# Performance work log

Measured on AMD Instinct MI355X. Metric: run time of the kernel, lower is better.

The kernel has to match this reference:

```python
import jax, jax.numpy as jnp
import numpy as np
from jax import lax

NUM_LABELS = 64  # groundtruth labels in [0, 64); label 0 = background (ignored in pair counts)


def _edges(H, W):
    # channel 0: edge (i,j)-(i+1,j); channel 1: edge (i,j)-(i,j+1)
    idx = np.arange(H * W).reshape(H, W)
    u0 = idx.copy(); v0 = np.roll(idx, -1, axis=0)
    u0[-1, :] = 0; v0[-1, :] = 0  # invalid boundary edges -> self edge, no-op
    u1 = idx.copy(); v1 = np.roll(idx, -1, axis=1)
    u1[:, -1] = 0; v1[:, -1] = 0
    u = np.concatenate([u0.ravel(), u1.ravel()]).astype(np.int32)
    v = np.concatenate([v0.ravel(), v1.ravel()]).astype(np.int32)
    return jnp.asarray(u), jnp.asarray(v)


def _find(parent, x, iters):
    # union-by-size keeps tree depth <= log2(N)+1, so a fixed number of hops suffices
    return lax.fori_loop(0, iters, lambda i, p: parent[p], x)


def _npairs(order, u, v, labels, pos):
    """Kruskal over edges sorted by descending affinity; for each merging edge,
    count pairs of voxels for which it is the maximin edge (pos: same nonzero
    label; neg: different nonzero labels). Pure int computation (non-diff)."""
    N = labels.shape[0]
    iters = int(np.ceil(np.log2(N))) + 2
    parent0 = jnp.arange(N, dtype=jnp.int32)
    size0 = jnp.ones(N, jnp.int32)
    counts0 = jax.nn.one_hot(labels, NUM_LABELS, dtype=jnp.int32)  # [N, L] label histogram per root

    def step(carry, e):
        parent, size, counts = carry
        ru = _find(parent, u[e], iters)
        rv = _find(parent, v[e], iters)
        cu = counts[ru]; cv = counts[rv]
        same = jnp.dot(cu[1:], cv[1:])          # same-nonzero-label pairs
        tu = cu[1:].sum(); tv = cv[1:].sum()    # nonzero-label voxel counts
        n = same if pos else tu * tv - same     # differing-label pairs for neg pass
        merge = ru != rv
        n = jnp.where(merge, n, 0)
        big = jnp.where(size[ru] >= size[rv], ru, rv)
        small = ru + rv - big
        parent = parent.at[small].set(jnp.where(merge, big, parent[small]))
        size = size.at[big].add(jnp.where(merge, size[small], 0))
        counts = counts.at[big].add(jnp.where(merge, counts[small], 0))
        return (parent, size, counts), n

    _, n = lax.scan(step, (parent0, size0, counts0), order)
    return n  # [E] int32, aligned with sorted order


def _malis_grad(aff, labels, u, v):
    # aff [E] float, labels [N] int. MALIS pseudo-loss gradients:
    # pos pass grad_e = n_pos_e * (a_e - 1); neg pass grad_e = n_neg_e * a_e;
    # combined = -(pos + neg) / 2 (as in MalisLoss.forward).
    order = jnp.argsort(-lax.stop_gradient(aff)).astype(jnp.int32)
    a_sorted = aff[order]
    n_pos = _npairs(order, u, v, labels, True).astype(aff.dtype)
    n_neg = _npairs(order, u, v, labels, False).astype(aff.dtype)
    g_sorted = n_pos * (a_sorted - 1.0) + n_neg * a_sorted
    return jnp.zeros_like(aff).at[order].set(-0.5 * g_sorted)


def setup_inputs() -> dict:
    key = jax.random.key(0)
    k1, k2 = jax.random.split(key)
    affinities = jax.random.uniform(k1, (2, 2, 128, 128), dtype=jnp.float32)
    groundtruth = jax.random.randint(k2, (2, 128, 128), 0, NUM_LABELS, dtype=jnp.int64)
    return {"affinities": affinities, "groundtruth": groundtruth}


def reference(affinities, groundtruth):
    B, C, H, W = affinities.shape
    u, v = _edges(H, W)
    aff = affinities.reshape(B, C * H * W)
    lab = groundtruth.reshape(B, H * W).astype(jnp.int32)
    grads = jax.vmap(lambda a, l: _malis_grad(a, l, u, v))(aff, lab)
    return grads.sum()  # pseudo_loss
```

## Files before the change

kernel.cpp:

```cpp
#include <hip/hip_runtime.h>

#define HDIM 128
#define WDIM 128
#define NPIX (HDIM * WDIM)
#define NEDGE (2 * NPIX)
#define BANDS 256
#define MAXK 256

typedef unsigned long long ull;

__device__ __forceinline__ void decode_edge(unsigned e, int& u, int& v) {
  if (e >= (unsigned)NEDGE) { u = 0; v = 0; return; }
  if (e < NPIX) {
    if (e < NPIX - WDIM) { u = (int)e; v = (int)e + WDIM; } else { u = 0; v = 0; }
  } else {
    unsigned t2 = e - NPIX;
    if ((t2 & (WDIM - 1)) != (WDIM - 1)) { u = (int)t2; v = (int)t2 + 1; } else { u = 0; v = 0; }
  }
}

__device__ __forceinline__ int bucket_of(float a) {
  int f = (int)(a * 256.0f);
  f = f < 0 ? 0 : (f > 255 ? 255 : f);
  return 255 - f;
}

__device__ __forceinline__ int cc_find(volatile unsigned* p, int x) {
  int px = (int)p[x];
  while (px != x) {
    int g = (int)p[px];
    if (g != px) p[x] = (unsigned)g;
    x = px; px = g;
  }
  return x;
}

__device__ __forceinline__ void uf_find2(unsigned* pn, int x, int y,
                                         int& rx, int& ry,
                                         unsigned& nzx, unsigned& nzy) {
  unsigned wx = pn[x];
  unsigned wy = pn[y];
  while (true) {
    int px = (int)(wx & 0xFFFFu);
    int py = (int)(wy & 0xFFFFu);
    bool mx = (px != x);
    bool my = (py != y);
    if (!mx && !my) break;
    if (mx) {
      unsigned wpx = pn[px];
      int gx = (int)(wpx & 0xFFFFu);
      if (gx != px) { pn[x] = (wx & 0xFFFF0000u) | (unsigned)gx; x = gx; wx = pn[gx]; }
      else { x = px; wx = wpx; }
    }
    if (my) {
      unsigned wpy = pn[py];
      int gy = (int)(wpy & 0xFFFFu);
      if (gy != py) { pn[y] = (wy & 0xFFFF0000u) | (unsigned)gy; y = gy; wy = pn[gy]; }
      else { y = py; wy = wpy; }
    }
  }
  rx = x; ry = y; nzx = wx >> 16; nzy = wy >> 16;
}

__device__ __forceinline__ ull shflx64(ull x, int m) {
  int lo = __shfl_xor((int)(unsigned)x, m, 64);
  int hi = __shfl_xor((int)(unsigned)(x >> 32), m, 64);
  return ((ull)(unsigned)hi << 32) | (unsigned)lo;
}

__global__ __launch_bounds__(1024) void band_kernel(const int* __restrict__ gt,
                                                    const float* __restrict__ aff_g,
                                                    float* __restrict__ out) {
  __shared__ unsigned pn[NPIX];
  __shared__ ull skbuf[MAXK];
  __shared__ unsigned scnt;
  const int img = blockIdx.x / BANDS;
  const int braw = blockIdx.x % BANDS;
  const int band = (img & 1) ? (BANDS - 1 - braw) : braw;
  const int* lab = gt + (size_t)img * NPIX;
  const float* aff = aff_g + (size_t)img * NEDGE;
  const int tid = threadIdx.x;

  if (band == 0) {
    if (tid < 64) pn[tid] = 0;
    __syncthreads();
    for (int i = tid; i < NPIX; i += 1024) atomicAdd(&pn[(unsigned)lab[i] & 63u], 1u);
    __syncthreads();
    if (tid == 0) {
      double s = 0.0;
      for (int l = 1; l < 64; ++l) { double m = (double)pn[l]; s += m * (m - 1.0) * 0.5; }
      atomicAdd(out, (float)(0.5 * s));
    }
    __syncthreads();
  }

  for (int i = tid; i < NPIX / 4; i += 1024) {
    uint4 w; w.x = 4u * i; w.y = 4u * i + 1u; w.z = 4u * i + 2u; w.w = 4u * i + 3u;
    ((uint4*)pn)[i] = w;
  }
  if (tid == 0) scnt = 0;
  __syncthreads();

  volatile unsigned* vp = pn;
  const float4* aff4 = (const float4*)aff;
  for (int t4 = tid; t4 < NEDGE / 4; t4 += 1024) {
    const float4 q = aff4[t4];
#pragma unroll
    for (int s = 0; s < 4; ++s) {
      const float a = (s == 0) ? q.x : (s == 1) ? q.y : (s == 2) ? q.z : q.w;
      const int b = bucket_of(a);
      if (b > band) continue;
      const unsigned e = (unsigned)(t4 * 4 + s);
      int u, v; decode_edge(e, u, v);
      if (u == v) continue;
      if (b == band) {
        unsigned bits = __float_as_uint(a);
        unsigned ob = (bits & 0x80000000u) ? ~bits : (bits | 0x80000000u);
        unsigned pos = atomicAdd(&scnt, 1u);
        if (pos < MAXK) skbuf[pos] = ((ull)(~ob) << 32) | e;
      } else {
        while (true) {
          int ru = cc_find(vp, u), rv = cc_find(vp, v);
          if (ru == rv) break;
          if (ru < rv) { int t = ru; ru = rv; rv = t; }
          unsigned old = atomicCAS(&pn[ru], (unsigned)ru, (unsigned)rv);
          if (old == (unsigned)ru) break;
          u = ru; v = rv;
        }
      }
    }
  }
  __syncthreads();
  unsigned cnt = scnt; if (cnt > MAXK) cnt = MAXK;

  ull myv[4];
  if (tid < 64) {
    const int lane = tid;
#pragma unroll
    for (int r = 0; r < 4; ++r) {
      unsigned idx = (unsigned)(r * 64 + lane);
      myv[r] = (idx < cnt) ? skbuf[idx] : ~0ull;
    }
#pragma unroll
    for (unsigned k = 2; k <= 256; k <<= 1) {
#pragma unroll
      for (unsigned j = k >> 1; j; j >>= 1) {
        if (j >= 64) {
          const int rj = (int)(j >> 6);
#pragma unroll
          for (int r = 0; r < 4; ++r) {
            if (!(r & rj)) {
              const int p = r | rj;
              const bool dir = ((((unsigned)r << 6) & k) == 0);
              ull a0 = myv[r], a1 = myv[p];
              if ((a0 > a1) == dir) { myv[r] = a1; myv[p] = a0; }
            }
          }
        } else {
#pragma unroll
          for (int r = 0; r < 4; ++r) {
            ull pv = shflx64(myv[r], (int)j);
            const bool low = ((lane & (int)j) == 0);
            const bool dir = (((((unsigned)r << 6) | (unsigned)lane) & k) == 0);
            const bool takemin = (low == dir);
            const bool less = (myv[r] < pv);
            myv[r] = (less == takemin) ? myv[r] : pv;
          }
        }
      }
    }
  } else {
    const int t = tid - 64;
    int prev = -1; unsigned acc = 0; bool multi = false;
    for (int k = 0; k < 18; ++k) {
      int i = t + k * 960;
      if (i >= NPIX) break;
      int r = i; unsigned p;
      while (((p = vp[r]) & 0xFFFFu) != (unsigned)r) r = (int)(p & 0xFFFFu);
      if (i != r) pn[i] = (unsigned)r;
      unsigned c = (lab[i] != 0) ? 1u : 0u;
      if (r != prev) {
        if (prev >= 0) { if (acc) atomicAdd(&pn[prev], acc << 16); multi = true; }
        prev = r; acc = c;
      } else {
        acc += c;
      }
    }
    const int wl = tid & 63;
    int first = __shfl(prev, 0);
    bool uni = __all(!multi && prev == first);
    if (uni) {
      unsigned s = acc;
      for (int off = 32; off; off >>= 1) s += __shfl_down(s, off);
      if (wl == 0 && s) atomicAdd(&pn[prev], s << 16);
    } else if (acc) {
      atomicAdd(&pn[prev], acc << 16);
    }
  }
  __syncthreads();

  if (tid < 64) {
    const int lane = tid;
    double acc = 0.0;
#pragma unroll
    for (int b8 = 0; b8 < 4; ++b8) {
      if ((unsigned)(b8 * 64) >= cnt) break;
      const ull myk_b = myv[b8];
      unsigned e = (unsigned)myk_b;
      unsigned khi = (unsigned)(myk_b >> 32);
      int u, v; decode_edge(e, u, v);
      const bool valid = (u != v);
      unsigned ob = ~khi;
      unsigned bits = (ob & 0x80000000u) ? (ob & 0x7FFFFFFFu) : ~ob;
      const float a = __uint_as_float(bits);

      int ru, rv; unsigned nzu, nzv;
      uf_find2(pn, u, v, ru, rv, nzu, nzv);

      unsigned long long m = __ballot(valid && (ru != rv));
      int myW = 0, myL = 0; unsigned snap = 0;
      while (m) {
        const int j = (int)(__ffsll(m) - 1);
        m &= m - 1;
        const int ruj = __builtin_amdgcn_readlane(ru, j);
        const int rvj = __builtin_amdgcn_readlane(rv, j);
        const unsigned nzuj = (unsigned)__builtin_amdgcn_readlane((int)nzu, j);
        const unsigned nzvj = (unsigned)__builtin_amdgcn_readlane((int)nzv, j);
        const bool live = (ruj != rvj);
        const unsigned mnz = nzuj + nzvj;
        int W = (nzuj >= nzvj) ? ruj : rvj;
        int L = ruj + rvj - W;
        W = live ? W : -1;
        L = live ? L : -1;
        const int sj = live ? j : 64;
        const unsigned spk = nzuj | (nzvj << 16);
        const bool turn = (lane == sj);
        if (turn) { myW = W; myL = L; snap = spk; }
        const bool uW = (ru == W), uL = (ru == L);
        const bool vW = (rv == W), vL = (rv == L);
        if (uL) ru = W;
        if (uW | uL) nzu = mnz;
        if (vL) rv = W;
        if (vW | vL) nzv = mnz;
      }
      pn[u] = (unsigned)ru;
      pn[v] = (unsigned)rv;
      if (myW != myL) {
        pn[myL] = (unsigned)myW;
        acc += (double)((snap & 0xFFFFu) * (snap >> 16)) * (double)a;
      }
      pn[ru] = (nzu << 16) | (unsigned)ru;
      pn[rv] = (nzv << 16) | (unsigned)rv;
    }
    for (int off = 32; off > 0; off >>= 1) acc += __shfl_down(acc, off);
    if (lane == 0) atomicAdd(out, (float)(-0.5 * acc));
  }
}

extern "C" void kernel_launch(void* const* d_in, const int* in_sizes, int n_in,
                              void* d_out, int out_size, void* d_ws, size_t ws_size,
                              hipStream_t stream) {
  const float* aff = (const float*)d_in[0];
  const int* gt = (const int*)d_in[1];
  float* out = (float*)d_out;
  const int B = in_sizes[1] / NPIX;

  hipMemsetAsync(d_out, 0, sizeof(float) * (size_t)out_size, stream);
  band_kernel<<<dim3(B * BANDS), dim3(1024), 0, stream>>>(gt, aff, out);
}
```

Baseline: 131.7 us.

## Pre-bucket edges by affinity band so each band block reads only lower bands

Measured after the change: 120.6 us. 8.4% less time.

```diff
diff --git a/kernel.cpp b/kernel.cpp
--- a/kernel.cpp
+++ b/kernel.cpp
@@ -23,6 +23,68 @@
   int f = (int)(a * 256.0f);
   f = f < 0 ? 0 : (f > 255 ? 255 : f);
   return 255 - f;
+}
+
+
+__global__ __launch_bounds__(1024) void hist_kernel(const float* __restrict__ aff_g,
+                                                    unsigned* __restrict__ ghist) {
+  __shared__ unsigned h[BANDS];
+  const int img = blockIdx.x >> 5;
+  const int slice = blockIdx.x & 31;
+  const int tid = threadIdx.x;
+  if (tid < BANDS) h[tid] = 0;
+  __syncthreads();
+  const unsigned e = (unsigned)(slice * 1024 + tid);
+  const float a = aff_g[(size_t)img * NEDGE + e];
+  int u, v; decode_edge(e, u, v);
+  if (u != v) atomicAdd(&h[bucket_of(a)], 1u);
+  __syncthreads();
+  if (tid < BANDS && h[tid]) atomicAdd(&ghist[img * BANDS + tid], h[tid]);
+}
+
+__global__ __launch_bounds__(1024) void scatter_kernel(const float* __restrict__ aff_g,
+                                                       const unsigned* __restrict__ ghist,
+                                                       unsigned* __restrict__ gcur,
+                                                       unsigned* __restrict__ gbase,
+                                                       ull* __restrict__ keys_g,
+                                                       unsigned* __restrict__ uv_g,
+                                                       float* __restrict__ out, int out_n) {
+  __shared__ unsigned hb[BANDS];
+  __shared__ unsigned lh[BANDS];
+  __shared__ unsigned go[BANDS];
+  const int img = blockIdx.x >> 5;
+  const int slice = blockIdx.x & 31;
+  const int tid = threadIdx.x;
+  if (blockIdx.x == 0 && tid < out_n) out[tid] = 0.f;
+  if (tid < BANDS) { hb[tid] = ghist[img * BANDS + tid]; lh[tid] = 0; }
+  __syncthreads();
+  for (int off = 1; off < BANDS; off <<= 1) {
+    unsigned vv = 0;
+    if (tid < BANDS && tid >= off) vv = hb[tid - off];
+    __syncthreads();
+    if (tid < BANDS) hb[tid] += vv;
+    __syncthreads();
+  }
+  const unsigned e = (unsigned)(slice * 1024 + tid);
+  const float a = aff_g[(size_t)img * NEDGE + e];
+  int u, v; decode_edge(e, u, v);
+  int b = -1; unsigned lpos = 0;
+  if (u != v) { b = bucket_of(a); lpos = atomicAdd(&lh[b], 1u); }
+  __syncthreads();
+  if (tid < BANDS && lh[tid]) go[tid] = atomicAdd(&gcur[img * BANDS + tid], lh[tid]);
+  if (slice == 0) {
+    if (tid < BANDS) gbase[img * (BANDS + 1) + tid] = (tid == 0) ? 0u : hb[tid - 1];
+    if (tid == 0) gbase[img * (BANDS + 1) + BANDS] = hb[BANDS - 1];
+  }
+  __syncthreads();
+  if (b >= 0) {
+    const unsigned base = (b == 0) ? 0u : hb[b - 1];
+    const unsigned pos = base + go[b] + lpos;
+    unsigned bits = __float_as_uint(a);
+    unsigned ob = (bits & 0x80000000u) ? ~bits : (bits | 0x80000000u);
+    keys_g[(size_t)img * NEDGE + pos] = ((ull)(~ob) << 32) | e;
+    uv_g[(size_t)img * NEDGE + pos] = ((unsigned)u << 16) | (unsigned)v;
+  }
 }
 
 __device__ __forceinline__ int cc_find(volatile unsigned* p, int x) {
@@ -69,17 +131,22 @@
 }
 
 __global__ __launch_bounds__(1024) void band_kernel(const int* __restrict__ gt,
-                                                    const float* __restrict__ aff_g,
+                                                    const ull* __restrict__ keys_g,
+                                                    const unsigned* __restrict__ uv_g,
+                                                    const unsigned* __restrict__ gbase,
                                                     float* __restrict__ out) {
   __shared__ unsigned pn[NPIX];
   __shared__ ull skbuf[MAXK];
-  __shared__ unsigned scnt;
   const int img = blockIdx.x / BANDS;
   const int braw = blockIdx.x % BANDS;
   const int band = (img & 1) ? (BANDS - 1 - braw) : braw;
   const int* lab = gt + (size_t)img * NPIX;
-  const float* aff = aff_g + (size_t)img * NEDGE;
+  const ull* keys = keys_g + (size_t)img * NEDGE;
+  const unsigned* uvp = uv_g + (size_t)img * NEDGE;
   const int tid = threadIdx.x;
+  const unsigned bstart = gbase[img * (BANDS + 1) + band];
+  const unsigned bend   = gbase[img * (BANDS + 1) + band + 1];
+  unsigned cnt = bend - bstart; if (cnt > MAXK) cnt = MAXK;
 
   if (band == 0) {
     if (tid < 64) pn[tid] = 0;
@@ -98,40 +165,23 @@
     uint4 w; w.x = 4u * i; w.y = 4u * i + 1u; w.z = 4u * i + 2u; w.w = 4u * i + 3u;
     ((uint4*)pn)[i] = w;
   }
-  if (tid == 0) scnt = 0;
+  if (tid < (int)cnt) skbuf[tid] = keys[bstart + tid];
   __syncthreads();
 
   volatile unsigned* vp = pn;
-  const float4* aff4 = (const float4*)aff;
-  for (int t4 = tid; t4 < NEDGE / 4; t4 += 1024) {
-    const float4 q = aff4[t4];
-#pragma unroll
-    for (int s = 0; s < 4; ++s) {
-      const float a = (s == 0) ? q.x : (s == 1) ? q.y : (s == 2) ? q.z : q.w;
-      const int b = bucket_of(a);
-      if (b > band) continue;
-      const unsigned e = (unsigned)(t4 * 4 + s);
-      int u, v; decode_edge(e, u, v);
-      if (u == v) continue;
-      if (b == band) {
-        unsigned bits = __float_as_uint(a);
-        unsigned ob = (bits & 0x80000000u) ? ~bits : (bits | 0x80000000u);
-        unsigned pos = atomicAdd(&scnt, 1u);
-        if (pos < MAXK) skbuf[pos] = ((ull)(~ob) << 32) | e;
-      } else {
-        while (true) {
-          int ru = cc_find(vp, u), rv = cc_find(vp, v);
-          if (ru == rv) break;
-          if (ru < rv) { int t = ru; ru = rv; rv = t; }
-          unsigned old = atomicCAS(&pn[ru], (unsigned)ru, (unsigned)rv);
-          if (old == (unsigned)ru) break;
-          u = ru; v = rv;
-        }
-      }
-    }
-  }
-  __syncthreads();
-  unsigned cnt = scnt; if (cnt > MAXK) cnt = MAXK;
+  for (unsigned i = tid; i < bstart; i += 1024) {
+    const unsigned p = uvp[i];
+    int u = (int)(p >> 16), v = (int)(p & 0xFFFFu);
+    while (true) {
+      int ru = cc_find(vp, u), rv = cc_find(vp, v);
+      if (ru == rv) break;
+      if (ru < rv) { int t = ru; ru = rv; rv = t; }
+      unsigned old = atomicCAS(&pn[ru], (unsigned)ru, (unsigned)rv);
+      if (old == (unsigned)ru) break;
+      u = ru; v = rv;
+    }
+  }
+  __syncthreads();
 
   ull myv[4];
   if (tid < 64) {
@@ -265,6 +315,15 @@
   float* out = (float*)d_out;
   const int B = in_sizes[1] / NPIX;
 
-  hipMemsetAsync(d_out, 0, sizeof(float) * (size_t)out_size, stream);
-  band_kernel<<<dim3(B * BANDS), dim3(1024), 0, stream>>>(gt, aff, out);
-}
+  ull* keys = (ull*)d_ws;
+  unsigned* uvp = (unsigned*)(keys + (size_t)B * NEDGE);
+  unsigned* ghist = uvp + (size_t)B * NEDGE;
+  unsigned* gcur = ghist + (size_t)B * BANDS;
+  unsigned* gbase = gcur + (size_t)B * BANDS;
+
+  hipMemsetAsync(ghist, 0, sizeof(unsigned) * 2 * (size_t)B * BANDS, stream);
+  hist_kernel<<<dim3(B * 32), dim3(1024), 0, stream>>>(aff, ghist);
+  scatter_kernel<<<dim3(B * 32), dim3(1024), 0, stream>>>(aff, ghist, gcur, gbase,
+                                                          keys, uvp, out, out_size);
+  band_kernel<<<dim3(B * BANDS), dim3(1024), 0, stream>>>(gt, keys, uvp, gbase, out);
+}
```
